# Kernel optimization log

Measured on AMD Instinct MI355X. Metric: run time of the kernel, lower is better.

Reference implementation:

```python
import jax, jax.numpy as jnp
import numpy as np
from jax import lax

B, L, C_IN, H = 2048, 128, 150, 230  # batch, seq_len, 3*word_size, hidden_size

MASK_TABLE = jnp.array([[0., 0., 0.],
                        [1., 0., 0.],
                        [0., 1., 0.],
                        [0., 0., 1.]], dtype=jnp.float32)  # frozen mask embedding


def setup_inputs() -> dict:
    key = jax.random.key(0)
    k1, k2, k3 = jax.random.split(key, 3)
    Xea = jax.random.normal(k1, (B, L, C_IN), dtype=jnp.float32)
    X_mask = jax.random.randint(k2, (B, L), 0, 4)
    # xavier_uniform for Conv1d weight [out, in, kw]
    fan_in, fan_out = C_IN * 3, H * 3
    limit = float(np.sqrt(6.0 / (fan_in + fan_out)))
    W = jax.random.uniform(k3, (H, C_IN, 3), dtype=jnp.float32, minval=-limit, maxval=limit)
    b = jnp.zeros((H,), dtype=jnp.float32)
    return {"Xea": Xea, "X_mask": X_mask, "W": W, "b": b}


def reference(Xea, X_mask, W, b):
    # Xea: [B, L, C_in] -> conv over sequence dim, kernel=3, padding=1
    x = jnp.transpose(Xea, (0, 2, 1))  # [B, C_in, L]
    y = lax.conv_general_dilated(
        x, W, window_strides=(1,), padding=[(1, 1)],
        dimension_numbers=('NCH', 'OIH', 'NCH'))  # [B, H, L]
    y = y + b[None, :, None]
    X = jnp.transpose(y, (0, 2, 1))  # [B, L, H]
    m = MASK_TABLE[X_mask]  # [B, L, 3] one-hot piece indicators (0 row = pad)
    # piecewise max pool: broadcast multiply then max over seq
    pooled = jnp.max(m[:, :, None, :] * X[:, :, :, None], axis=1)  # [B, H, 3]
    return jnp.tanh(pooled.reshape(pooled.shape[0], -1))  # [B, 3*H]
```

## Files before the change

kernel.cpp:

```cpp
#include <hip/hip_runtime.h>
#include <hip/hip_bf16.h>
#include <math.h>


#define B_SZ   2048
#define L_SEQ  128
#define C_INCH 150
#define H_OUT  230
#define RS     152
#define NROW   129
#define NS8    2451

typedef __attribute__((ext_vector_type(8))) short short8;
typedef __attribute__((ext_vector_type(4))) float float4v;

static __device__ __forceinline__ unsigned short f2bf(float f) {
    union { float f; unsigned u; } x{f};
    unsigned r = (x.u + 0x7FFFu + ((x.u >> 16) & 1u)) >> 16;
    return (unsigned short)r;
}

static __device__ __forceinline__ unsigned cvt2(float2 f) {
    __hip_bfloat162 h = __float22bfloat162_rn(f);
    union { __hip_bfloat162 h; unsigned u; } c{h};
    return c.u;
}

static __device__ __forceinline__ float tanh_fast_pos(float v) {
    float e = __expf(2.0f * v);
    return 1.0f - 2.0f / (e + 1.0f);
}

static __device__ __forceinline__ void gl_lds16(const void* g, void* l) {
    __builtin_amdgcn_global_load_lds(
        (const __attribute__((address_space(1))) unsigned int*)g,
        (__attribute__((address_space(3))) unsigned int*)l, 16, 0, 0);
}

__global__ void pack_w_kernel(const float* __restrict__ W,
                              unsigned short* __restrict__ Wpk) {
    int t = blockIdx.x * 256 + threadIdx.x;
    int kk   = t >> 10;
    int rem  = t & 1023;
    int ht   = rem >> 6;
    int lane = rem & 63;
    int q    = lane >> 4;
    int c15  = lane & 15;
    int k    = kk / 5;
    int kc   = kk - k * 5;
    int h    = ht * 16 + c15;
    int cb   = kc * 32 + q * 8;
    unsigned short v[8];
    #pragma unroll
    for (int e = 0; e < 8; ++e) {
        int c = cb + e;
        float f = (h < H_OUT && c < C_INCH) ? W[h * 450 + c * 3 + k] : 0.0f;
        v[e] = f2bf(f);
    }
    *(short8*)(Wpk + (size_t)t * 8) = *(short8*)v;
}

__global__ void __launch_bounds__(512, 4)
pcnn_mfma(const float* __restrict__ Xea, const int* __restrict__ Xmask,
          const unsigned short* __restrict__ Wpk,
          const float* __restrict__ bias, float* __restrict__ out) {
    __shared__ __align__(16) unsigned short sX[NROW * RS];
    __shared__ __align__(16) float sSel[L_SEQ * 3];
    __shared__ __align__(1024) unsigned char sB[2 * 16384];

    const int b    = blockIdx.x;
    const int tid  = threadIdx.x;
    const int wv   = tid >> 6;
    const int lane = tid & 63;
    const int q    = lane >> 4;
    const int c15  = lane & 15;
    const int mh   = wv & 1;
    const int nh   = wv >> 1;

    const char* wsrc = (const char*)Wpk;
    const int ub = wv * 2048;
    const int lo = ub + lane * 16;

    gl_lds16(wsrc + lo,        (char*)sB + ub);
    gl_lds16(wsrc + lo + 1024, (char*)sB + ub + 1024);

    const float* xb = Xea + (size_t)b * (L_SEQ * C_INCH);
    float2 pl[5][4];
    #pragma unroll
    for (int it = 0; it < 5; ++it) {
        const int t   = it * 512 + tid;
        const int tc  = (t < NS8) ? t : (NS8 - 1);
        const int row = tc / 19;
        const int j   = tc - row * 19;
        const int rm1 = (row > 0) ? (row - 1) : 0;
        const float* s = xb + rm1 * C_INCH + j * 8;
        pl[it][0] = *(const float2*)(s);
        pl[it][1] = *(const float2*)(s + 2);
        pl[it][2] = *(const float2*)(s + 4);
        pl[it][3] = *(const float2*)(s + ((j < 18) ? 6 : 4));
    }

    if (tid < L_SEQ) {
        int mv = Xmask[(size_t)b * L_SEQ + tid];
        sSel[tid * 3 + 0] = (mv == 1) ? 0.0f : -1e30f;
        sSel[tid * 3 + 1] = (mv == 2) ? 0.0f : -1e30f;
        sSel[tid * 3 + 2] = (mv == 3) ? 0.0f : -1e30f;
    }

    #pragma unroll
    for (int it = 0; it < 5; ++it) {
        const int t   = it * 512 + tid;
        const int tc  = (t < NS8) ? t : (NS8 - 1);
        const int row = tc / 19;
        const int j   = tc - row * 19;
        uint4 u;
        u.x = cvt2(pl[it][0]);
        u.y = cvt2(pl[it][1]);
        u.z = cvt2(pl[it][2]);
        u.w = cvt2(pl[it][3]);
        const bool z = (row == 0);
        u.x = z ? 0u : u.x;
        u.y = z ? 0u : u.y;
        u.z = z ? 0u : u.z;
        u.w = (z || j == 18) ? 0u : u.w;
        if (t < NS8) *(uint4*)(sX + (size_t)t * 8) = u;
    }

    __syncthreads();

    float4v acc[4][4];
    #pragma unroll
    for (int mi = 0; mi < 4; ++mi)
        #pragma unroll
        for (int nj = 0; nj < 4; ++nj)
            acc[mi][nj] = (float4v){0.f, 0.f, 0.f, 0.f};

    const unsigned short* a0p = sX + (mh * 64 + c15) * RS + q * 8;
    const unsigned short* a3p2 = (mh == 1 && c15 == 15) ? (a0p - 129 * RS) : a0p;

    const int bfo = (nh * 4) * 1024 + lane * 16;

    #pragma unroll
    for (int kk = 0; kk < 15; ++kk) {
        const int buf = kk & 1;
        if (kk < 14) {
            const char* src = wsrc + (size_t)(kk + 1) * 16384;
            char* dst = (char*)sB + (buf ^ 1) * 16384;
            gl_lds16(src + lo,        dst + ub);
            gl_lds16(src + lo + 1024, dst + ub + 1024);
        }
        const int k  = kk / 5;
        const int kc = kk - k * 5;

        const char* bbase = (const char*)sB + buf * 16384 + bfo;
        short8 bfrag[4];
        #pragma unroll
        for (int nj = 0; nj < 4; ++nj)
            bfrag[nj] = *(const short8*)(bbase + nj * 1024);

        short8 a[4];
        #pragma unroll
        for (int mi = 0; mi < 4; ++mi) {
            const unsigned short* base = (mi == 3 && k == 2) ? a3p2 : a0p;
            a[mi] = *(const short8*)(base + (mi * 16 + k) * RS + kc * 32);
        }
        #pragma unroll
        for (int mi = 0; mi < 4; ++mi)
            #pragma unroll
            for (int nj = 0; nj < 4; ++nj)
                acc[mi][nj] = __builtin_amdgcn_mfma_f32_16x16x32_bf16(
                    a[mi], bfrag[nj], acc[mi][nj], 0, 0, 0);

        if (kk < 14) __syncthreads();
    }

    float pz[4][3];
    #pragma unroll
    for (int nj = 0; nj < 4; ++nj)
        #pragma unroll
        for (int p = 0; p < 3; ++p) pz[nj][p] = -1e30f;

    #pragma unroll
    for (int mi = 0; mi < 4; ++mi) {
        const int l0 = mh * 64 + mi * 16 + q * 4;
        const float4v* sp = (const float4v*)(sSel + l0 * 3);
        const float4v s0 = sp[0], s1 = sp[1], s2 = sp[2];
        const float sl[12] = {s0.x, s0.y, s0.z, s0.w, s1.x, s1.y,
                              s1.z, s1.w, s2.x, s2.y, s2.z, s2.w};
        #pragma unroll
        for (int nj = 0; nj < 4; ++nj)
            #pragma unroll
            for (int r = 0; r < 4; ++r) {
                const float y = acc[mi][nj][r];
                pz[nj][0] = fmaxf(pz[nj][0], y + sl[r * 3 + 0]);
                pz[nj][1] = fmaxf(pz[nj][1], y + sl[r * 3 + 1]);
                pz[nj][2] = fmaxf(pz[nj][2], y + sl[r * 3 + 2]);
            }
    }

    __syncthreads();
    float* sP = (float*)sX;

    #pragma unroll
    for (int nj = 0; nj < 4; ++nj) {
        float p0 = pz[nj][0], p1 = pz[nj][1], p2 = pz[nj][2];
        p0 = fmaxf(p0, __shfl_xor(p0, 16, 64));
        p1 = fmaxf(p1, __shfl_xor(p1, 16, 64));
        p2 = fmaxf(p2, __shfl_xor(p2, 16, 64));
        p0 = fmaxf(p0, __shfl_xor(p0, 32, 64));
        p1 = fmaxf(p1, __shfl_xor(p1, 32, 64));
        p2 = fmaxf(p2, __shfl_xor(p2, 32, 64));
        if (q == 0) {
            const int hl = nh * 64 + nj * 16 + c15;
            float* d = sP + (mh * 256 + hl) * 3;
            d[0] = p0; d[1] = p1; d[2] = p2;
        }
    }
    __syncthreads();

    for (int t = tid; t < 768; t += 512) {
        const int h = t / 3;
        const int p = t - h * 3;
        if (h < H_OUT) {
            float v = fmaxf(sP[h * 3 + p], sP[(256 + h) * 3 + p]);
            v = fmaxf(0.0f, v + bias[h]);
            out[(size_t)b * (3 * H_OUT) + h * 3 + p] = tanh_fast_pos(v);
        }
    }
}

extern "C" void kernel_launch(void* const* d_in, const int* in_sizes, int n_in,
                              void* d_out, int out_size, void* d_ws, size_t ws_size,
                              hipStream_t stream) {
    const float* Xea   = (const float*)d_in[0];
    const int*   Xmask = (const int*)d_in[1];
    const float* W     = (const float*)d_in[2];
    const float* bias  = (const float*)d_in[3];
    float* out = (float*)d_out;
    unsigned short* Wpk = (unsigned short*)d_ws;

    pack_w_kernel<<<60, 256, 0, stream>>>(W, Wpk);
    pcnn_mfma<<<B_SZ, 512, 0, stream>>>(Xea, Xmask, Wpk, bias, out);
}
```

Measured before the change: 267.2 us.

## Load weight fragments directly into registers, drop LDS staging and barriers

Weight B-fragments are now read straight from global memory (L2-resident packed weights) into a register double buffer instead of being staged in LDS with global_load_lds. This removes the 32KB LDS buffer and the per-k-step __syncthreads, which should allow more occupancy and fewer stalls. It also raises wave priority around the MFMA block and adds sched barriers. In exchange each wave issues its own global loads, so L2 traffic rises and latency is hidden only by a one-step register prefetch.

```diff
diff --git a/kernel.cpp b/kernel.cpp
--- a/kernel.cpp
+++ b/kernel.cpp
@@ -29,12 +29,6 @@
 static __device__ __forceinline__ float tanh_fast_pos(float v) {
     float e = __expf(2.0f * v);
     return 1.0f - 2.0f / (e + 1.0f);
-}
-
-static __device__ __forceinline__ void gl_lds16(const void* g, void* l) {
-    __builtin_amdgcn_global_load_lds(
-        (const __attribute__((address_space(1))) unsigned int*)g,
-        (__attribute__((address_space(3))) unsigned int*)l, 16, 0, 0);
 }
 
 __global__ void pack_w_kernel(const float* __restrict__ W,
@@ -66,7 +60,6 @@
           const float* __restrict__ bias, float* __restrict__ out) {
     __shared__ __align__(16) unsigned short sX[NROW * RS];
     __shared__ __align__(16) float sSel[L_SEQ * 3];
-    __shared__ __align__(1024) unsigned char sB[2 * 16384];
 
     const int b    = blockIdx.x;
     const int tid  = threadIdx.x;
@@ -77,12 +70,12 @@
     const int mh   = wv & 1;
     const int nh   = wv >> 1;
 
-    const char* wsrc = (const char*)Wpk;
-    const int ub = wv * 2048;
-    const int lo = ub + lane * 16;
-
-    gl_lds16(wsrc + lo,        (char*)sB + ub);
-    gl_lds16(wsrc + lo + 1024, (char*)sB + ub + 1024);
+    const unsigned short* wp = Wpk + ((size_t)(nh * 4) * 64 + lane) * 8;
+
+    short8 bb[2][4];
+    #pragma unroll
+    for (int nj = 0; nj < 4; ++nj)
+        bb[0][nj] = *(const short8*)(wp + nj * 512);
 
     const float* xb = Xea + (size_t)b * (L_SEQ * C_INCH);
     float2 pl[5][4];
@@ -138,40 +131,32 @@
     const unsigned short* a0p = sX + (mh * 64 + c15) * RS + q * 8;
     const unsigned short* a3p2 = (mh == 1 && c15 == 15) ? (a0p - 129 * RS) : a0p;
 
-    const int bfo = (nh * 4) * 1024 + lane * 16;
-
     #pragma unroll
     for (int kk = 0; kk < 15; ++kk) {
-        const int buf = kk & 1;
+        const int cur = kk & 1;
         if (kk < 14) {
-            const char* src = wsrc + (size_t)(kk + 1) * 16384;
-            char* dst = (char*)sB + (buf ^ 1) * 16384;
-            gl_lds16(src + lo,        dst + ub);
-            gl_lds16(src + lo + 1024, dst + ub + 1024);
+            #pragma unroll
+            for (int nj = 0; nj < 4; ++nj)
+                bb[cur ^ 1][nj] =
+                    *(const short8*)(wp + (size_t)(kk + 1) * 8192 + nj * 512);
         }
         const int k  = kk / 5;
         const int kc = kk - k * 5;
-
-        const char* bbase = (const char*)sB + buf * 16384 + bfo;
-        short8 bfrag[4];
-        #pragma unroll
-        for (int nj = 0; nj < 4; ++nj)
-            bfrag[nj] = *(const short8*)(bbase + nj * 1024);
-
         short8 a[4];
         #pragma unroll
         for (int mi = 0; mi < 4; ++mi) {
             const unsigned short* base = (mi == 3 && k == 2) ? a3p2 : a0p;
             a[mi] = *(const short8*)(base + (mi * 16 + k) * RS + kc * 32);
         }
+        __builtin_amdgcn_s_setprio(1);
         #pragma unroll
         for (int mi = 0; mi < 4; ++mi)
             #pragma unroll
             for (int nj = 0; nj < 4; ++nj)
                 acc[mi][nj] = __builtin_amdgcn_mfma_f32_16x16x32_bf16(
-                    a[mi], bfrag[nj], acc[mi][nj], 0, 0, 0);
-
-        if (kk < 14) __syncthreads();
+                    a[mi], bb[cur][nj], acc[mi][nj], 0, 0, 0);
+        __builtin_amdgcn_s_setprio(0);
+        __builtin_amdgcn_sched_barrier(0);
     }
 
     float pz[4][3];
```

Result: faster. 256.3 us (-4.1%).
